# Optimization experiments

Hardware: AMD Instinct MI355X
Metric: run time of the kernel (lower is better)

## Reference

```python
import jax, jax.numpy as jnp
import numpy as np

N, E, ET = 100000, 1000000, 200000
F, D, H, L = 64, 32, 66, 2
BN_EPS = 1e-5

def _w(key, shape):
    fan_in = shape[-2] if len(shape) >= 2 else shape[-1]
    return jax.random.normal(key, shape, dtype=jnp.float32) / np.sqrt(fan_in)

def setup_inputs() -> dict:
    key = jax.random.key(0)
    ks = jax.random.split(key, 30)
    inp = {
        'x': jax.random.normal(ks[0], (N, F), dtype=jnp.float32),
        'edge_index': jax.random.randint(ks[1], (2, E), 0, N),
        'edge_attr': jax.random.normal(ks[2], (E, D), dtype=jnp.float32),
        'edge_label_index': jax.random.randint(ks[3], (2, ET), 0, N),
        'target_edge_attr': jax.random.normal(ks[4], (ET, D), dtype=jnp.float32),
        # embeddings
        'node_w': _w(ks[5], (F, H)), 'node_b': jnp.zeros((H,), jnp.float32),
        'edge_w': _w(ks[6], (D, H)), 'edge_b': jnp.zeros((H,), jnp.float32),
        # per-layer GINEConv MLP (Linear-ReLU-Linear), stacked over layers
        'conv_w1': _w(ks[7], (L, H, H)), 'conv_b1': jnp.zeros((L, H), jnp.float32),
        'conv_w2': _w(ks[8], (L, H, H)), 'conv_b2': jnp.zeros((L, H), jnp.float32),
        # per-layer BatchNorm affine params
        'bn_gamma': jnp.ones((L, H), jnp.float32), 'bn_beta': jnp.zeros((L, H), jnp.float32),
        # per-layer edge-update MLP (3H -> H -> H)
        'emlp_w1': _w(ks[9], (L, 3 * H, H)), 'emlp_b1': jnp.zeros((L, H), jnp.float32),
        'emlp_w2': _w(ks[10], (L, H, H)), 'emlp_b2': jnp.zeros((L, H), jnp.float32),
        # final classifier MLP (3H -> 50 -> 25 -> 2); dropout treated as eval (identity)
        'mlp_w1': _w(ks[11], (3 * H, 50)), 'mlp_b1': jnp.zeros((50,), jnp.float32),
        'mlp_w2': _w(ks[12], (50, 25)), 'mlp_b2': jnp.zeros((25,), jnp.float32),
        'mlp_w3': _w(ks[13], (25, 2)), 'mlp_b3': jnp.zeros((2,), jnp.float32),
    }
    return inp

def reference(x, edge_attr, target_edge_attr, node_w, node_b, edge_w, edge_b,
              conv_w1, conv_b1, conv_w2, conv_b2, bn_gamma, bn_beta,
              emlp_w1, emlp_b1, emlp_w2, emlp_b2,
              mlp_w1, mlp_b1, mlp_w2, mlp_b2, mlp_w3, mlp_b3,
              edge_index, edge_label_index):
    n = x.shape[0]
    src, dst = edge_index[0], edge_index[1]
    tsrc, tdst = edge_label_index[0], edge_label_index[1]
    h = x @ node_w + node_b              # [N, H]
    ea = edge_attr @ edge_w + edge_b     # [E, H]
    tea = target_edge_attr @ edge_w + edge_b  # [ET, H]
    n_layers = conv_w1.shape[0]
    for i in range(n_layers):
        # GINEConv: (1+eps)*x + sum_j relu(x_j + e_ij), eps=0, then MLP
        msg = jax.nn.relu(h[src] + ea)                               # [E, H]
        aggr = jax.ops.segment_sum(msg, dst, num_segments=n)         # [N, H]
        z = h + aggr
        z = jax.nn.relu(z @ conv_w1[i] + conv_b1[i]) @ conv_w2[i] + conv_b2[i]
        # BatchNorm (training-mode batch stats, biased variance)
        mean = z.mean(axis=0)
        var = jnp.var(z, axis=0)
        z = (z - mean) * jax.lax.rsqrt(var + BN_EPS) * bn_gamma[i] + bn_beta[i]
        h = (h + jax.nn.relu(z)) / 2
        # edge update on target edges
        cat = jnp.concatenate([h[tsrc], h[tdst], tea], axis=-1)      # [ET, 3H]
        upd = jax.nn.relu(cat @ emlp_w1[i] + emlp_b1[i]) @ emlp_w2[i] + emlp_b2[i]
        tea = tea + upd / 2
    pair = jax.nn.relu(jnp.concatenate([h[tsrc], h[tdst]], axis=-1))  # [ET, 2H]
    feat = jnp.concatenate([pair, tea], axis=-1)                      # [ET, 3H]
    o = jax.nn.relu(feat @ mlp_w1 + mlp_b1)
    o = jax.nn.relu(o @ mlp_w2 + mlp_b2)
    return o @ mlp_w3 + mlp_b3
```

## Files before the change

### kernel.cpp

```cpp
#include <hip/hip_runtime.h>

#define NN 100000
#define NE 1000000
#define NT 200000
#define SCB 391

typedef __attribute__((ext_vector_type(8))) short short8;
typedef __attribute__((ext_vector_type(4))) float f32x4;

__device__ __forceinline__ unsigned short f2b(float x) {
  union { float f; unsigned int u; } v; v.f = x;
  unsigned int r = v.u + 0x7fffu + ((v.u >> 16) & 1u);
  return (unsigned short)(r >> 16);
}
__device__ __forceinline__ float b2f(unsigned short x) {
  union { unsigned int u; float f; } v; v.u = ((unsigned int)x) << 16;
  return v.f;
}

struct PrepTab {
  const float* a[14]; const float* b[14];
  int K[14], C[14], rows[14], off[14];
};

__global__ __launch_bounds__(256) void prep_w(PrepTab tab, unsigned short* wT) {
  int s = blockIdx.x;
  const float* A = tab.a[s];
  const float* B = tab.b[s];
  int K = tab.K[s], C = tab.C[s], rows = tab.rows[s];
  unsigned short* dst = wT + tab.off[s];
  int n = rows * 104;
  for (int i = threadIdx.x; i < n; i += 256) {
    int c = i / 104, k = i - c * 104;
    float v = 0.0f;
    if (k < K) {
      if (c < C) v = A[k * C + c];
      else if (B && c < 2 * C) v = B[k * C + (c - C)];
    }
    dst[i] = f2b(v);
  }
}

template<int K, int KSTEPS, int CT, int C, int AIN, int ROUT>
__global__ __launch_bounds__(256) void mfma_gemm(
    const void* __restrict__ in, const float* __restrict__ add,
    const unsigned short* __restrict__ Bt, const float* __restrict__ bias,
    void* __restrict__ outp, void* __restrict__ out2, int R)
{
  constexpr int CR = CT * 16;
  __shared__ __align__(16) unsigned short As[64 * 104];
  __shared__ __align__(16) unsigned short Bs[CR * 104];
  __shared__ float bs[CR];
  const int t = threadIdx.x;
  const int r0 = blockIdx.x * 64;
  for (int i = t; i < CT * 208; i += 256) ((uint4*)Bs)[i] = ((const uint4*)Bt)[i];
  if (t < CR) bs[t] = (bias && t < C) ? bias[t] : 0.0f;
  constexpr int KH = KSTEPS * 16;
  for (int i = t; i < 64 * KH; i += 256) {
    int r = i / KH, kk = (i - r * KH) * 2;
    int rg = r0 + r;
    unsigned short u0 = 0, u1 = 0;
    if (rg < R && kk < K) {
      if constexpr (AIN == 3) {
        unsigned int u = ((const unsigned int*)in)[((size_t)rg * K + kk) >> 1];
        u0 = u & 0xffffu; u1 = u >> 16;
      } else {
        float2 f = *(const float2*)((const float*)in + (size_t)rg * K + kk);
        float v0 = f.x, v1 = f.y;
        if constexpr (AIN == 1) {
          float2 g = *(const float2*)(add + (size_t)rg * K + kk);
          v0 += g.x; v1 += g.y;
        }
        if constexpr (AIN == 2) { v0 = fmaxf(v0, 0.f); v1 = fmaxf(v1, 0.f); }
        u0 = f2b(v0); u1 = f2b(v1);
      }
    }
    As[r * 104 + kk] = u0; As[r * 104 + kk + 1] = u1;
  }
  __syncthreads();
  const int lane = t & 63, w = t >> 6, m = lane & 15, q = lane >> 4;
  f32x4 acc[CT] = {};
  const unsigned short* Ap = As + (w * 16 + m) * 104 + q * 8;
  const unsigned short* Bp = Bs + m * 104 + q * 8;
#pragma unroll
  for (int ks = 0; ks < KSTEPS; ks++) {
    short8 a = *(const short8*)(Ap + ks * 32);
#pragma unroll
    for (int ct = 0; ct < CT; ct++) {
      short8 b = *(const short8*)(Bp + ct * 16 * 104 + ks * 32);
      acc[ct] = __builtin_amdgcn_mfma_f32_16x16x32_bf16(a, b, acc[ct], 0, 0, 0);
    }
  }
#pragma unroll
  for (int ct = 0; ct < CT; ct++) {
    int c = ct * 16 + m;
    if (c < C) {
      float bv = bs[c];
#pragma unroll
      for (int r2 = 0; r2 < 4; r2++) {
        int row = r0 + w * 16 + q * 4 + r2;
        if (row < R) {
          float v = acc[ct][r2] + bv;
          if constexpr ((ROUT & 1) != 0) v = fmaxf(v, 0.f);
          if constexpr ((ROUT & 2) != 0)
            ((unsigned short*)outp)[(size_t)row * C + c] = f2b(v);
          else
            ((float*)outp)[(size_t)row * C + c] = v;
          if constexpr ((ROUT & 4) != 0)
            ((unsigned short*)out2)[(size_t)row * C + c] = f2b(v);
        }
      }
    }
  }
}

__global__ __launch_bounds__(256) void hist_kernel(const int* __restrict__ ei,
                                                   int* __restrict__ deg)
{
  int e = blockIdx.x * 256 + threadIdx.x;
  if (e < NE) atomicAdd(&deg[ei[NE + e]], 1);
}

__global__ __launch_bounds__(256) void blocksum_k(const int* __restrict__ deg,
                                                  int* __restrict__ bsum)
{
  __shared__ int red[256];
  const int t = threadIdx.x;
  int i = blockIdx.x * 256 + t;
  red[t] = (i < NN) ? deg[i] : 0;
  __syncthreads();
  for (int s = 128; s > 0; s >>= 1) {
    if (t < s) red[t] += red[t + s];
    __syncthreads();
  }
  if (t == 0) bsum[blockIdx.x] = red[0];
}

__global__ __launch_bounds__(512) void scansums_k(int* __restrict__ bsum,
                                                  int* __restrict__ rowptr)
{
  __shared__ int s[512];
  const int t = threadIdx.x;
  s[t] = (t < SCB) ? bsum[t] : 0;
  __syncthreads();
  for (int off = 1; off < 512; off <<= 1) {
    int v = (t >= off) ? s[t - off] : 0;
    __syncthreads();
    s[t] += v;
    __syncthreads();
  }
  if (t < SCB) bsum[t] = (t == 0) ? 0 : s[t - 1];
  if (t == 0) rowptr[NN] = NE;
}

__global__ __launch_bounds__(256) void scatter_scan_k(
    const int* __restrict__ deg, const int* __restrict__ bsum,
    int* __restrict__ rowptr)
{
  __shared__ int s[256];
  const int t = threadIdx.x;
  int i = blockIdx.x * 256 + t;
  int v = (i < NN) ? deg[i] : 0;
  s[t] = v;
  __syncthreads();
  for (int off = 1; off < 256; off <<= 1) {
    int x = (t >= off) ? s[t - off] : 0;
    __syncthreads();
    s[t] += x;
    __syncthreads();
  }
  if (i < NN) rowptr[i] = bsum[blockIdx.x] + s[t] - v;
}

__global__ __launch_bounds__(256) void fill_kernel(
    const int* __restrict__ ei, const int* __restrict__ rowptr,
    int* __restrict__ cur, int* __restrict__ srcS, int* __restrict__ dstS,
    int* __restrict__ permS, int* __restrict__ invp)
{
  int e = blockIdx.x * 256 + threadIdx.x;
  if (e >= NE) return;
  int d = ei[NE + e];
  int pos = atomicAdd(&cur[d], 1);
  int w = rowptr[d] + pos;
  srcS[w] = ei[e];
  dstS[w] = d;
  permS[w] = e;
  invp[e] = w;
}

__global__ __launch_bounds__(256) void perm_eattr(
    const float* __restrict__ eattr, const int* __restrict__ invp,
    unsigned short* __restrict__ eaB)
{
  int i = blockIdx.x * 256 + threadIdx.x;
  if (i >= NE * 16) return;
  int e = i >> 4, j = i & 15;
  float2 f = ((const float2*)eattr)[i];
  unsigned int packed = (unsigned int)f2b(f.x) | ((unsigned int)f2b(f.y) << 16);
  ((unsigned int*)eaB)[(size_t)invp[e] * 16 + j] = packed;
}

__global__ __launch_bounds__(256) void msg_aggr2(
    const int* __restrict__ rowptr, const int* __restrict__ srcS,
    const int* __restrict__ dstS, const unsigned short* __restrict__ eaB,
    const float* __restrict__ eattr, const int* __restrict__ permS,
    const unsigned short* __restrict__ Bt, const float* __restrict__ bias,
    const unsigned short* __restrict__ hB, float* __restrict__ aggr)
{
  __shared__ __align__(16) unsigned short As[64 * 40];
  __shared__ __align__(16) unsigned short Bs[80 * 104];
  __shared__ float msgS[64 * 67];
  __shared__ float bs[80];
  __shared__ int sidx[64], didx[64];
  __shared__ int runStart[65];
  __shared__ int nrunsS;
  const int t = threadIdx.x;
  const int e0 = blockIdx.x * 64;
  for (int i = t; i < 1040; i += 256) ((uint4*)Bs)[i] = ((const uint4*)Bt)[i];
  if (t < 80) bs[t] = (t < 66) ? bias[t] : 0.0f;
  if (t < 64) { sidx[t] = srcS[e0 + t]; didx[t] = dstS[e0 + t]; }
  if (eaB) {
    for (int i = t; i < 1024; i += 256) {
      int r = i >> 4, j = i & 15;
      unsigned int u = ((const unsigned int*)eaB)[(size_t)(e0 + r) * 16 + j];
      As[r * 40 + j * 2] = u & 0xffffu;
      As[r * 40 + j * 2 + 1] = u >> 16;
    }
  } else {
    for (int i = t; i < 1024; i += 256) {
      int r = i >> 4, j = i & 15;
      int p = permS[e0 + r];
      float2 f = ((const float2*)(eattr + (size_t)p * 32))[j];
      As[r * 40 + j * 2] = f2b(f.x);
      As[r * 40 + j * 2 + 1] = f2b(f.y);
    }
  }
  __syncthreads();
  if (t < 64) {
    bool b = (t == 0) || (didx[t] != didx[t - 1]);
    unsigned long long mask = __ballot(b);
    int idx = __popcll(mask & ((1ull << t) - 1ull));
    if (b) runStart[idx] = t;
    if (t == 63) { nrunsS = __popcll(mask); runStart[__popcll(mask)] = 64; }
  }
  const int lane = t & 63, w = t >> 6, m = lane & 15, q = lane >> 4;
  f32x4 acc[5] = {};
  short8 a = *(const short8*)(As + (w * 16 + m) * 40 + q * 8);
#pragma unroll
  for (int ct = 0; ct < 5; ct++) {
    short8 b = *(const short8*)(Bs + (ct * 16 + m) * 104 + q * 8);
    acc[ct] = __builtin_amdgcn_mfma_f32_16x16x32_bf16(a, b, acc[ct], 0, 0, 0);
  }
#pragma unroll
  for (int ct = 0; ct < 5; ct++) {
    int c = ct * 16 + m;
    if (c < 66) {
      float bv = bs[c];
#pragma unroll
      for (int r2 = 0; r2 < 4; r2++) {
        int e = w * 16 + q * 4 + r2;
        float v = acc[ct][r2] + bv + b2f(hB[(size_t)sidx[e] * 66 + c]);
        msgS[e * 67 + c] = fmaxf(v, 0.f);
      }
    }
  }
  __syncthreads();
  const int nr = nrunsS;
  for (int task = t; task < nr * 66; task += 256) {
    int r = task / 66, c = task - r * 66;
    int s0 = runStart[r], s1 = runStart[r + 1];
    float s = 0.0f;
    for (int e = s0; e < s1; e++) s += msgS[e * 67 + c];
    int n = didx[s0];
    bool partial = false;
    if (r == 0)      partial = (rowptr[n] < e0);
    if (r == nr - 1) partial = partial || (rowptr[n + 1] > e0 + 64);
    if (partial) atomicAdd(&aggr[(size_t)n * 66 + c], s);
    else         aggr[(size_t)n * 66 + c] = s;
  }
}

__global__ __launch_bounds__(256) void bn_stats(const float* __restrict__ z,
                                                float* __restrict__ stat)
{
  const int t = threadIdx.x;
  if (t >= 198) return;
  const int c = t % 66, rs = t / 66;
  const int r0 = blockIdx.x * 1024;
  float s1 = 0.0f, s2 = 0.0f;
  int rend = r0 + 1024; if (rend > NN) rend = NN;
  for (int r = r0 + rs; r < rend; r += 3) {
    float v = z[(size_t)r * 66 + c];
    s1 += v; s2 += v * v;
  }
  atomicAdd(&stat[c], s1);
  atomicAdd(&stat[66 + c], s2);
}

__global__ __launch_bounds__(256) void bn_update(
    float* __restrict__ h, unsigned short* __restrict__ hB,
    const float* __restrict__ z, const float* __restrict__ stat,
    const float* __restrict__ gamma, const float* __restrict__ beta)
{
  int idx = blockIdx.x * 256 + threadIdx.x;
  if (idx >= NN * 66) return;
  int c = idx % 66;
  float mean = stat[c] * (1.0f / NN);
  float var  = stat[66 + c] * (1.0f / NN) - mean * mean;
  float inv  = rsqrtf(var + 1e-5f);
  float zn   = (z[idx] - mean) * inv * gamma[c] + beta[c];
  float v = 0.5f * (h[idx] + fmaxf(zn, 0.0f));
  h[idx] = v;
  hB[idx] = f2b(v);
}

__global__ __launch_bounds__(256) void edge_fused2(
    const float* __restrict__ P12, const int* __restrict__ eli,
    const unsigned short* __restrict__ B1t, const float* __restrict__ b1,
    const unsigned short* __restrict__ B2t, const float* __restrict__ b2,
    float* __restrict__ tea)
{
  __shared__ __align__(16) unsigned short As[64 * 104];
  __shared__ __align__(16) unsigned short Bs1[80 * 104];
  __shared__ __align__(16) unsigned short Bs2[80 * 104];
  __shared__ float b1s[80], b2s[80];
  __shared__ int sidx[64], didx[64];
  const int t = threadIdx.x;
  const int e0 = blockIdx.x * 64;
  for (int i = t; i < 1040; i += 256) {
    ((uint4*)Bs1)[i] = ((const uint4*)B1t)[i];
    ((uint4*)Bs2)[i] = ((const uint4*)B2t)[i];
  }
  if (t < 80) { b1s[t] = (t < 66) ? b1[t] : 0.f; b2s[t] = (t < 66) ? b2[t] : 0.f; }
  if (t < 64) { sidx[t] = eli[e0 + t]; didx[t] = eli[NT + e0 + t]; }
  for (int i = t; i < 64 * 48; i += 256) {
    int r = i / 48, kk = (i - r * 48) * 2;
    unsigned short u0 = 0, u1 = 0;
    if (kk < 66) {
      float2 f = *(const float2*)(tea + (size_t)(e0 + r) * 66 + kk);
      u0 = f2b(f.x); u1 = f2b(f.y);
    }
    As[r * 104 + kk] = u0; As[r * 104 + kk + 1] = u1;
  }
  __syncthreads();
  const int lane = t & 63, w = t >> 6, m = lane & 15, q = lane >> 4;
  const unsigned short* Ap = As + (w * 16 + m) * 104 + q * 8;
  const unsigned short* Bp1 = Bs1 + m * 104 + q * 8;
  f32x4 acc[5] = {};
#pragma unroll
  for (int ks = 0; ks < 3; ks++) {
    short8 a = *(const short8*)(Ap + ks * 32);
#pragma unroll
    for (int ct = 0; ct < 5; ct++) {
      short8 b = *(const short8*)(Bp1 + ct * 16 * 104 + ks * 32);
      acc[ct] = __builtin_amdgcn_mfma_f32_16x16x32_bf16(a, b, acc[ct], 0, 0, 0);
    }
  }
  __syncthreads();
#pragma unroll
  for (int ct = 0; ct < 5; ct++) {
    int c = ct * 16 + m;
    if (c < 66) {
      float bv = b1s[c];
#pragma unroll
      for (int r2 = 0; r2 < 4; r2++) {
        int e = w * 16 + q * 4 + r2;
        float v = acc[ct][r2] + bv + P12[(size_t)sidx[e] * 132 + c]
                                   + P12[(size_t)didx[e] * 132 + 66 + c];
        As[e * 104 + c] = f2b(fmaxf(v, 0.f));
      }
    }
  }
  __syncthreads();
  const unsigned short* Bp2 = Bs2 + m * 104 + q * 8;
  f32x4 acc2[5] = {};
#pragma unroll
  for (int ks = 0; ks < 3; ks++) {
    short8 a = *(const short8*)(Ap + ks * 32);
#pragma unroll
    for (int ct = 0; ct < 5; ct++) {
      short8 b = *(const short8*)(Bp2 + ct * 16 * 104 + ks * 32);
      acc2[ct] = __builtin_amdgcn_mfma_f32_16x16x32_bf16(a, b, acc2[ct], 0, 0, 0);
    }
  }
#pragma unroll
  for (int ct = 0; ct < 5; ct++) {
    int c = ct * 16 + m;
    if (c < 66) {
      float bv = b2s[c];
#pragma unroll
      for (int r2 = 0; r2 < 4; r2++) {
        int e = w * 16 + q * 4 + r2;
        size_t idx = (size_t)(e0 + e) * 66 + c;
        tea[idx] += 0.5f * (acc2[ct][r2] + bv);
      }
    }
  }
}

__global__ __launch_bounds__(256) void final_fused2(
    const float* __restrict__ tea, const float* __restrict__ P12f,
    const int* __restrict__ eli, const unsigned short* __restrict__ B1t,
    const float* __restrict__ b1, const float* __restrict__ w2,
    const float* __restrict__ b2, const float* __restrict__ w3,
    const float* __restrict__ b3, float* __restrict__ out)
{
  __shared__ __align__(16) unsigned short As[64 * 104];
  __shared__ __align__(16) unsigned short Bs[64 * 104];
  __shared__ float o1s[64 * 51];
  __shared__ float o2s[64 * 25];
  __shared__ float w2s[50 * 25], w3s[50];
  __shared__ float b1s[64], b2s[25], b3s[2];
  __shared__ int sidx[64], didx[64];
  const int t = threadIdx.x;
  const int e0 = blockIdx.x * 64;
  for (int i = t; i < 832; i += 256) ((uint4*)Bs)[i] = ((const uint4*)B1t)[i];
  for (int i = t; i < 50 * 25; i += 256) w2s[i] = w2[i];
  if (t < 50) w3s[t] = w3[t];
  if (t < 64) { b1s[t] = (t < 50) ? b1[t] : 0.f; sidx[t] = eli[e0 + t]; didx[t] = eli[NT + e0 + t]; }
  if (t < 25) b2s[t] = b2[t];
  if (t < 2)  b3s[t] = b3[t];
  for (int i = t; i < 64 * 48; i += 256) {
    int r = i / 48, kk = (i - r * 48) * 2;
    unsigned short u0 = 0, u1 = 0;
    if (kk < 66) {
      float2 f = *(const float2*)(tea + (size_t)(e0 + r) * 66 + kk);
      u0 = f2b(f.x); u1 = f2b(f.y);
    }
    As[r * 104 + kk] = u0; As[r * 104 + kk + 1] = u1;
  }
  __syncthreads();
  const int lane = t & 63, w = t >> 6, m = lane & 15, q = lane >> 4;
  const unsigned short* Ap = As + (w * 16 + m) * 104 + q * 8;
  const unsigned short* Bp = Bs + m * 104 + q * 8;
  f32x4 acc[4] = {};
#pragma unroll
  for (int ks = 0; ks < 3; ks++) {
    short8 a = *(const short8*)(Ap + ks * 32);
#pragma unroll
    for (int ct = 0; ct < 4; ct++) {
      short8 b = *(const short8*)(Bp + ct * 16 * 104 + ks * 32);
      acc[ct] = __builtin_amdgcn_mfma_f32_16x16x32_bf16(a, b, acc[ct], 0, 0, 0);
    }
  }
#pragma unroll
  for (int ct = 0; ct < 4; ct++) {
    int c = ct * 16 + m;
    if (c < 50) {
      float bv = b1s[c];
#pragma unroll
      for (int r2 = 0; r2 < 4; r2++) {
        int e = w * 16 + q * 4 + r2;
        float v = acc[ct][r2] + bv + P12f[(size_t)sidx[e] * 100 + c]
                                   + P12f[(size_t)didx[e] * 100 + 50 + c];
        o1s[e * 51 + c] = fmaxf(v, 0.f);
      }
    }
  }
  __syncthreads();
  for (int it = t; it < 64 * 25; it += 256) {
    int e = it / 25, c = it - e * 25;
    float s = b2s[c];
    for (int k = 0; k < 50; k++) s = fmaf(o1s[e * 51 + k], w2s[k * 25 + c], s);
    o2s[e * 25 + c] = fmaxf(s, 0.f);
  }
  __syncthreads();
  if (t < 128) {
    int e = t >> 1, c = t & 1;
    float s = b3s[c];
    for (int k = 0; k < 25; k++) s = fmaf(o2s[e * 25 + k], w3s[k * 2 + c], s);
    out[(size_t)(e0 + e) * 2 + c] = s;
  }
}

extern "C" void kernel_launch(void* const* d_in, const int* in_sizes, int n_in,
                              void* d_out, int out_size, void* d_ws, size_t ws_size,
                              hipStream_t stream) {
  const float* x      = (const float*)d_in[0];
  const int*   ei     = (const int*)  d_in[1];
  const float* eattr  = (const float*)d_in[2];
  const int*   eli    = (const int*)  d_in[3];
  const float* tattr  = (const float*)d_in[4];
  const float* node_w = (const float*)d_in[5];
  const float* node_b = (const float*)d_in[6];
  const float* edge_w = (const float*)d_in[7];
  const float* edge_b = (const float*)d_in[8];
  const float* cw1    = (const float*)d_in[9];
  const float* cb1    = (const float*)d_in[10];
  const float* cw2    = (const float*)d_in[11];
  const float* cb2    = (const float*)d_in[12];
  const float* bng    = (const float*)d_in[13];
  const float* bnb    = (const float*)d_in[14];
  const float* ew1    = (const float*)d_in[15];
  const float* eb1    = (const float*)d_in[16];
  const float* ew2    = (const float*)d_in[17];
  const float* eb2    = (const float*)d_in[18];
  const float* mw1    = (const float*)d_in[19];
  const float* mb1    = (const float*)d_in[20];
  const float* mw2    = (const float*)d_in[21];
  const float* mb2    = (const float*)d_in[22];
  const float* mw3    = (const float*)d_in[23];
  const float* mb3    = (const float*)d_in[24];
  float* out = (float*)d_out;

  char* p = (char*)d_ws;
  auto alloc = [&](size_t bytes) { void* r = p; p += (bytes + 255) & ~(size_t)255; return r; };
  float* h      = (float*)alloc((size_t)NN * 66 * 4);
  unsigned short* hB = (unsigned short*)alloc((size_t)NN * 66 * 2);
  float* big    = (float*)alloc((size_t)NN * 132 * 4);
  float* zbuf   = (float*)alloc((size_t)NN * 66 * 4);
  float* tea    = (float*)alloc((size_t)NT * 66 * 4);
  float* stat   = (float*)alloc(1024);
  int*   rowptr = (int*)alloc((NN + 1) * 4);
  int*   cur    = (int*)alloc((size_t)NN * 4);
  int*   bsum   = (int*)alloc((SCB + 1) * 4);
  int*   srcS   = (int*)alloc((size_t)NE * 4);
  int*   dstS   = (int*)alloc((size_t)NE * 4);
  int*   permS  = (int*)alloc((size_t)NE * 4);
  int*   invp   = (int*)alloc((size_t)NE * 4);
  unsigned short* wT = (unsigned short*)alloc((size_t)140000 * 2);
  size_t used = (size_t)(p - (char*)d_ws);
  unsigned short* eaB = nullptr;
  if (ws_size >= used + (size_t)NE * 32 * 2 + 256)
    eaB = (unsigned short*)alloc((size_t)NE * 32 * 2);

  const int gN = (NN + 63) / 64;
  const int gT = NT / 64;
  const int gE = NE / 64;

  hipMemsetAsync(cur, 0, (size_t)NN * sizeof(int), stream);
  hist_kernel<<<(NE + 255) / 256, 256, 0, stream>>>(ei, cur);
  blocksum_k<<<SCB, 256, 0, stream>>>(cur, bsum);
  scansums_k<<<1, 512, 0, stream>>>(bsum, rowptr);
  scatter_scan_k<<<SCB, 256, 0, stream>>>(cur, bsum, rowptr);
  hipMemsetAsync(cur, 0, (size_t)NN * sizeof(int), stream);
  fill_kernel<<<(NE + 255) / 256, 256, 0, stream>>>(ei, rowptr, cur, srcS, dstS, permS, invp);
  if (eaB)
    perm_eattr<<<(NE * 16 + 255) / 256, 256, 0, stream>>>(eattr, invp, eaB);

  PrepTab tb;
  int offs[14];
  int off = 0;
  auto set = [&](int s, const float* A, const float* B, int K, int C, int rows) {
    tb.a[s] = A; tb.b[s] = B; tb.K[s] = K; tb.C[s] = C; tb.rows[s] = rows;
    tb.off[s] = off; offs[s] = off; off += rows * 104;
  };
  set(0, node_w, nullptr, 64, 66, 80);
  set(1, edge_w, nullptr, 32, 66, 80);
  for (int l = 0; l < 2; l++) {
    set(2 + l, cw1 + (size_t)l * 4356, nullptr, 66, 66, 80);
    set(4 + l, cw2 + (size_t)l * 4356, nullptr, 66, 66, 80);
    set(6 + l, ew1 + (size_t)l * 13068 + 8712, nullptr, 66, 66, 80);
    set(8 + l, ew2 + (size_t)l * 4356, nullptr, 66, 66, 80);
    set(10 + l, ew1 + (size_t)l * 13068, ew1 + (size_t)l * 13068 + 4356,
        66, 66, 144);
  }
  set(12, mw1, mw1 + 3300, 66, 50, 112);
  set(13, mw1 + 6600, nullptr, 66, 50, 80);
  prep_w<<<14, 256, 0, stream>>>(tb, wT);

  mfma_gemm<64, 2, 5, 66, 0, 4><<<gN, 256, 0, stream>>>(
      x, nullptr, wT + offs[0], node_b, h, hB, NN);
  mfma_gemm<32, 1, 5, 66, 0, 0><<<gT, 256, 0, stream>>>(
      tattr, nullptr, wT + offs[1], edge_b, tea, nullptr, NT);

  for (int l = 0; l < 2; l++) {
    hipMemsetAsync(zbuf, 0, (size_t)NN * 66 * sizeof(float), stream);
    msg_aggr2<<<gE, 256, 0, stream>>>(rowptr, srcS, dstS, eaB, eattr, permS,
                                      wT + offs[1], edge_b, hB, zbuf);
    mfma_gemm<66, 3, 5, 66, 1, 3><<<gN, 256, 0, stream>>>(
        h, zbuf, wT + offs[2 + l], cb1 + l * 66, (unsigned short*)big, nullptr, NN);
    mfma_gemm<66, 3, 5, 66, 3, 0><<<gN, 256, 0, stream>>>(
        (unsigned short*)big, nullptr, wT + offs[4 + l], cb2 + l * 66, zbuf, nullptr, NN);
    hipMemsetAsync(stat, 0, 132 * sizeof(float), stream);
    bn_stats<<<(NN + 1023) / 1024, 256, 0, stream>>>(zbuf, stat);
    bn_update<<<(NN * 66 + 255) / 256, 256, 0, stream>>>(h, hB, zbuf, stat,
                                                         bng + l * 66, bnb + l * 66);
    mfma_gemm<66, 3, 9, 132, 0, 0><<<gN, 256, 0, stream>>>(
        h, nullptr, wT + offs[10 + l], nullptr, big, nullptr, NN);
    edge_fused2<<<gT, 256, 0, stream>>>(big, eli, wT + offs[6 + l], eb1 + l * 66,
                                        wT + offs[8 + l], eb2 + l * 66, tea);
  }

  mfma_gemm<66, 3, 7, 100, 2, 0><<<gN, 256, 0, stream>>>(
      h, nullptr, wT + offs[12], nullptr, big, nullptr, NN);
  final_fused2<<<gT, 256, 0, stream>>>(tea, big, eli, wT + offs[13], mb1,
                                       mw2, mb2, mw3, mb3, out);
}
```

Before: 1.284 ms.

## Precompute edge embeddings once and store per-node projections as bf16

```diff
diff --git a/kernel.cpp b/kernel.cpp
--- a/kernel.cpp
+++ b/kernel.cpp
@@ -200,25 +200,18 @@
   ((unsigned int*)eaB)[(size_t)invp[e] * 16 + j] = packed;
 }
 
-__global__ __launch_bounds__(256) void msg_aggr2(
-    const int* __restrict__ rowptr, const int* __restrict__ srcS,
-    const int* __restrict__ dstS, const unsigned short* __restrict__ eaB,
-    const float* __restrict__ eattr, const int* __restrict__ permS,
-    const unsigned short* __restrict__ Bt, const float* __restrict__ bias,
-    const unsigned short* __restrict__ hB, float* __restrict__ aggr)
+__global__ __launch_bounds__(256) void eaw_kernel(
+    const unsigned short* __restrict__ eaB, const float* __restrict__ eattr,
+    const int* __restrict__ permS, const unsigned short* __restrict__ Bt,
+    const float* __restrict__ bias, unsigned short* __restrict__ eaW)
 {
   __shared__ __align__(16) unsigned short As[64 * 40];
   __shared__ __align__(16) unsigned short Bs[80 * 104];
-  __shared__ float msgS[64 * 67];
   __shared__ float bs[80];
-  __shared__ int sidx[64], didx[64];
-  __shared__ int runStart[65];
-  __shared__ int nrunsS;
   const int t = threadIdx.x;
   const int e0 = blockIdx.x * 64;
   for (int i = t; i < 1040; i += 256) ((uint4*)Bs)[i] = ((const uint4*)Bt)[i];
   if (t < 80) bs[t] = (t < 66) ? bias[t] : 0.0f;
-  if (t < 64) { sidx[t] = srcS[e0 + t]; didx[t] = dstS[e0 + t]; }
   if (eaB) {
     for (int i = t; i < 1024; i += 256) {
       int r = i >> 4, j = i & 15;
@@ -236,6 +229,41 @@
     }
   }
   __syncthreads();
+  const int lane = t & 63, w = t >> 6, m = lane & 15, q = lane >> 4;
+  f32x4 acc[5] = {};
+  short8 a = *(const short8*)(As + (w * 16 + m) * 40 + q * 8);
+#pragma unroll
+  for (int ct = 0; ct < 5; ct++) {
+    short8 b = *(const short8*)(Bs + (ct * 16 + m) * 104 + q * 8);
+    acc[ct] = __builtin_amdgcn_mfma_f32_16x16x32_bf16(a, b, acc[ct], 0, 0, 0);
+  }
+#pragma unroll
+  for (int ct = 0; ct < 5; ct++) {
+    int c = ct * 16 + m;
+    if (c < 66) {
+      float bv = bs[c];
+#pragma unroll
+      for (int r2 = 0; r2 < 4; r2++) {
+        int e = w * 16 + q * 4 + r2;
+        eaW[(size_t)(e0 + e) * 66 + c] = f2b(acc[ct][r2] + bv);
+      }
+    }
+  }
+}
+
+__global__ __launch_bounds__(256) void msg_aggr3(
+    const int* __restrict__ rowptr, const int* __restrict__ srcS,
+    const int* __restrict__ dstS, const unsigned int* __restrict__ eaW32,
+    const unsigned int* __restrict__ hB32, float* __restrict__ aggr)
+{
+  __shared__ float msgS[64 * 67];
+  __shared__ int sidx[64], didx[64];
+  __shared__ int runStart[65];
+  __shared__ int nrunsS;
+  const int t = threadIdx.x;
+  const int e0 = blockIdx.x * 64;
+  if (t < 64) { sidx[t] = srcS[e0 + t]; didx[t] = dstS[e0 + t]; }
+  __syncthreads();
   if (t < 64) {
     bool b = (t == 0) || (didx[t] != didx[t - 1]);
     unsigned long long mask = __ballot(b);
@@ -243,26 +271,14 @@
     if (b) runStart[idx] = t;
     if (t == 63) { nrunsS = __popcll(mask); runStart[__popcll(mask)] = 64; }
   }
-  const int lane = t & 63, w = t >> 6, m = lane & 15, q = lane >> 4;
-  f32x4 acc[5] = {};
-  short8 a = *(const short8*)(As + (w * 16 + m) * 40 + q * 8);
-#pragma unroll
-  for (int ct = 0; ct < 5; ct++) {
-    short8 b = *(const short8*)(Bs + (ct * 16 + m) * 104 + q * 8);
-    acc[ct] = __builtin_amdgcn_mfma_f32_16x16x32_bf16(a, b, acc[ct], 0, 0, 0);
-  }
-#pragma unroll
-  for (int ct = 0; ct < 5; ct++) {
-    int c = ct * 16 + m;
-    if (c < 66) {
-      float bv = bs[c];
-#pragma unroll
-      for (int r2 = 0; r2 < 4; r2++) {
-        int e = w * 16 + q * 4 + r2;
-        float v = acc[ct][r2] + bv + b2f(hB[(size_t)sidx[e] * 66 + c]);
-        msgS[e * 67 + c] = fmaxf(v, 0.f);
-      }
-    }
+  for (int idx = t; idx < 64 * 33; idx += 256) {
+    int e = idx / 33, j = idx - e * 33;
+    unsigned int ua = eaW32[(size_t)e0 * 33 + idx];
+    unsigned int uh = hB32[(size_t)sidx[e] * 33 + j];
+    float v0 = b2f((unsigned short)(ua & 0xffffu)) + b2f((unsigned short)(uh & 0xffffu));
+    float v1 = b2f((unsigned short)(ua >> 16)) + b2f((unsigned short)(uh >> 16));
+    msgS[e * 67 + 2 * j]     = fmaxf(v0, 0.f);
+    msgS[e * 67 + 2 * j + 1] = fmaxf(v1, 0.f);
   }
   __syncthreads();
   const int nr = nrunsS;
@@ -280,6 +296,86 @@
   }
 }
 
+__global__ __launch_bounds__(256) void msg_aggr2(
+    const int* __restrict__ rowptr, const int* __restrict__ srcS,
+    const int* __restrict__ dstS, const unsigned short* __restrict__ eaB,
+    const float* __restrict__ eattr, const int* __restrict__ permS,
+    const unsigned short* __restrict__ Bt, const float* __restrict__ bias,
+    const unsigned short* __restrict__ hB, float* __restrict__ aggr)
+{
+  __shared__ __align__(16) unsigned short As[64 * 40];
+  __shared__ __align__(16) unsigned short Bs[80 * 104];
+  __shared__ float msgS[64 * 67];
+  __shared__ float bs[80];
+  __shared__ int sidx[64], didx[64];
+  __shared__ int runStart[65];
+  __shared__ int nrunsS;
+  const int t = threadIdx.x;
+  const int e0 = blockIdx.x * 64;
+  for (int i = t; i < 1040; i += 256) ((uint4*)Bs)[i] = ((const uint4*)Bt)[i];
+  if (t < 80) bs[t] = (t < 66) ? bias[t] : 0.0f;
+  if (t < 64) { sidx[t] = srcS[e0 + t]; didx[t] = dstS[e0 + t]; }
+  if (eaB) {
+    for (int i = t; i < 1024; i += 256) {
+      int r = i >> 4, j = i & 15;
+      unsigned int u = ((const unsigned int*)eaB)[(size_t)(e0 + r) * 16 + j];
+      As[r * 40 + j * 2] = u & 0xffffu;
+      As[r * 40 + j * 2 + 1] = u >> 16;
+    }
+  } else {
+    for (int i = t; i < 1024; i += 256) {
+      int r = i >> 4, j = i & 15;
+      int p = permS[e0 + r];
+      float2 f = ((const float2*)(eattr + (size_t)p * 32))[j];
+      As[r * 40 + j * 2] = f2b(f.x);
+      As[r * 40 + j * 2 + 1] = f2b(f.y);
+    }
+  }
+  __syncthreads();
+  if (t < 64) {
+    bool b = (t == 0) || (didx[t] != didx[t - 1]);
+    unsigned long long mask = __ballot(b);
+    int idx = __popcll(mask & ((1ull << t) - 1ull));
+    if (b) runStart[idx] = t;
+    if (t == 63) { nrunsS = __popcll(mask); runStart[__popcll(mask)] = 64; }
+  }
+  const int lane = t & 63, w = t >> 6, m = lane & 15, q = lane >> 4;
+  f32x4 acc[5] = {};
+  short8 a = *(const short8*)(As + (w * 16 + m) * 40 + q * 8);
+#pragma unroll
+  for (int ct = 0; ct < 5; ct++) {
+    short8 b = *(const short8*)(Bs + (ct * 16 + m) * 104 + q * 8);
+    acc[ct] = __builtin_amdgcn_mfma_f32_16x16x32_bf16(a, b, acc[ct], 0, 0, 0);
+  }
+#pragma unroll
+  for (int ct = 0; ct < 5; ct++) {
+    int c = ct * 16 + m;
+    if (c < 66) {
+      float bv = bs[c];
+#pragma unroll
+      for (int r2 = 0; r2 < 4; r2++) {
+        int e = w * 16 + q * 4 + r2;
+        float v = acc[ct][r2] + bv + b2f(hB[(size_t)sidx[e] * 66 + c]);
+        msgS[e * 67 + c] = fmaxf(v, 0.f);
+      }
+    }
+  }
+  __syncthreads();
+  const int nr = nrunsS;
+  for (int task = t; task < nr * 66; task += 256) {
+    int r = task / 66, c = task - r * 66;
+    int s0 = runStart[r], s1 = runStart[r + 1];
+    float s = 0.0f;
+    for (int e = s0; e < s1; e++) s += msgS[e * 67 + c];
+    int n = didx[s0];
+    bool partial = false;
+    if (r == 0)      partial = (rowptr[n] < e0);
+    if (r == nr - 1) partial = partial || (rowptr[n + 1] > e0 + 64);
+    if (partial) atomicAdd(&aggr[(size_t)n * 66 + c], s);
+    else         aggr[(size_t)n * 66 + c] = s;
+  }
+}
+
 __global__ __launch_bounds__(256) void bn_stats(const float* __restrict__ z,
                                                 float* __restrict__ stat)
 {
@@ -315,7 +411,7 @@
 }
 
 __global__ __launch_bounds__(256) void edge_fused2(
-    const float* __restrict__ P12, const int* __restrict__ eli,
+    const unsigned short* __restrict__ P12, const int* __restrict__ eli,
     const unsigned short* __restrict__ B1t, const float* __restrict__ b1,
     const unsigned short* __restrict__ B2t, const float* __restrict__ b2,
     float* __restrict__ tea)
@@ -365,8 +461,8 @@
 #pragma unroll
       for (int r2 = 0; r2 < 4; r2++) {
         int e = w * 16 + q * 4 + r2;
-        float v = acc[ct][r2] + bv + P12[(size_t)sidx[e] * 132 + c]
-                                   + P12[(size_t)didx[e] * 132 + 66 + c];
+        float v = acc[ct][r2] + bv + b2f(P12[(size_t)sidx[e] * 132 + c])
+                                   + b2f(P12[(size_t)didx[e] * 132 + 66 + c]);
         As[e * 104 + c] = f2b(fmaxf(v, 0.f));
       }
     }
@@ -399,7 +495,7 @@
 }
 
 __global__ __launch_bounds__(256) void final_fused2(
-    const float* __restrict__ tea, const float* __restrict__ P12f,
+    const float* __restrict__ tea, const unsigned short* __restrict__ P12f,
     const int* __restrict__ eli, const unsigned short* __restrict__ B1t,
     const float* __restrict__ b1, const float* __restrict__ w2,
     const float* __restrict__ b2, const float* __restrict__ w3,
@@ -451,8 +547,8 @@
 #pragma unroll
       for (int r2 = 0; r2 < 4; r2++) {
         int e = w * 16 + q * 4 + r2;
-        float v = acc[ct][r2] + bv + P12f[(size_t)sidx[e] * 100 + c]
-                                   + P12f[(size_t)didx[e] * 100 + 50 + c];
+        float v = acc[ct][r2] + bv + b2f(P12f[(size_t)sidx[e] * 100 + c])
+                                   + b2f(P12f[(size_t)didx[e] * 100 + 50 + c]);
         o1s[e * 51 + c] = fmaxf(v, 0.f);
       }
     }
@@ -520,6 +616,10 @@
   int*   invp   = (int*)alloc((size_t)NE * 4);
   unsigned short* wT = (unsigned short*)alloc((size_t)140000 * 2);
   size_t used = (size_t)(p - (char*)d_ws);
+  unsigned short* eaW = nullptr;
+  if (ws_size >= used + (size_t)NE * 66 * 2 + 256)
+    eaW = (unsigned short*)alloc((size_t)NE * 66 * 2);
+  used = (size_t)(p - (char*)d_ws);
   unsigned short* eaB = nullptr;
   if (ws_size >= used + (size_t)NE * 32 * 2 + 256)
     eaB = (unsigned short*)alloc((size_t)NE * 32 * 2);
@@ -559,6 +659,9 @@
   set(13, mw1 + 6600, nullptr, 66, 50, 80);
   prep_w<<<14, 256, 0, stream>>>(tb, wT);
 
+  if (eaW)
+    eaw_kernel<<<gE, 256, 0, stream>>>(eaB, eattr, permS, wT + offs[1], edge_b, eaW);
+
   mfma_gemm<64, 2, 5, 66, 0, 4><<<gN, 256, 0, stream>>>(
       x, nullptr, wT + offs[0], node_b, h, hB, NN);
   mfma_gemm<32, 1, 5, 66, 0, 0><<<gT, 256, 0, stream>>>(
@@ -566,8 +669,13 @@
 
   for (int l = 0; l < 2; l++) {
     hipMemsetAsync(zbuf, 0, (size_t)NN * 66 * sizeof(float), stream);
-    msg_aggr2<<<gE, 256, 0, stream>>>(rowptr, srcS, dstS, eaB, eattr, permS,
-                                      wT + offs[1], edge_b, hB, zbuf);
+    if (eaW)
+      msg_aggr3<<<gE, 256, 0, stream>>>(rowptr, srcS, dstS,
+                                        (const unsigned int*)eaW,
+                                        (const unsigned int*)hB, zbuf);
+    else
+      msg_aggr2<<<gE, 256, 0, stream>>>(rowptr, srcS, dstS, eaB, eattr, permS,
+                                        wT + offs[1], edge_b, hB, zbuf);
     mfma_gemm<66, 3, 5, 66, 1, 3><<<gN, 256, 0, stream>>>(
         h, zbuf, wT + offs[2 + l], cb1 + l * 66, (unsigned short*)big, nullptr, NN);
     mfma_gemm<66, 3, 5, 66, 3, 0><<<gN, 256, 0, stream>>>(
@@ -576,14 +684,16 @@
     bn_stats<<<(NN + 1023) / 1024, 256, 0, stream>>>(zbuf, stat);
     bn_update<<<(NN * 66 + 255) / 256, 256, 0, stream>>>(h, hB, zbuf, stat,
                                                          bng + l * 66, bnb + l * 66);
-    mfma_gemm<66, 3, 9, 132, 0, 0><<<gN, 256, 0, stream>>>(
+    mfma_gemm<66, 3, 9, 132, 0, 2><<<gN, 256, 0, stream>>>(
         h, nullptr, wT + offs[10 + l], nullptr, big, nullptr, NN);
-    edge_fused2<<<gT, 256, 0, stream>>>(big, eli, wT + offs[6 + l], eb1 + l * 66,
+    edge_fused2<<<gT, 256, 0, stream>>>((const unsigned short*)big, eli,
+                                        wT + offs[6 + l], eb1 + l * 66,
                                         wT + offs[8 + l], eb2 + l * 66, tea);
   }
 
-  mfma_gemm<66, 3, 7, 100, 2, 0><<<gN, 256, 0, stream>>>(
+  mfma_gemm<66, 3, 7, 100, 2, 2><<<gN, 256, 0, stream>>>(
       h, nullptr, wT + offs[12], nullptr, big, nullptr, NN);
-  final_fused2<<<gT, 256, 0, stream>>>(tea, big, eli, wT + offs[13], mb1,
+  final_fused2<<<gT, 256, 0, stream>>>(tea, (const unsigned short*)big, eli,
+                                       wT + offs[13], mb1,
                                        mw2, mb2, mw3, mb3, out);
 }
```

New measurement: 1.280 ms. No clear change (-0.4%).
